# Optimization experiments

Hardware: AMD Instinct MI355X
Metric: run time of the kernel (lower is better)

The kernel has to match this reference:

```python
import jax, jax.numpy as jnp
import numpy as np
from math import factorial

LMAX = 2
MUL = 8            # output_size (mul_in1 = mul_in2)
MUL_OUT = 16       # channels_out
NBASIS = 16
MAX_RADIUS = 5.0
EMB_DIM = 16
MAX_ATOM = 10
N_NODES = 40000
N_EDGES = 500000
N_GRAPHS = 16

# ---- real Clebsch-Gordan coefficients (computed once in numpy) ----

def _cg_coef(j1, m1, j2, m2, j3, m3):
    if m1 + m2 != m3:
        return 0.0
    f = factorial
    pre = ((2 * j3 + 1) * f(j3 + j1 - j2) * f(j3 - j1 + j2) * f(j1 + j2 - j3) / f(j1 + j2 + j3 + 1)) ** 0.5
    pre *= (f(j3 + m3) * f(j3 - m3) * f(j1 - m1) * f(j1 + m1) * f(j2 - m2) * f(j2 + m2)) ** 0.5
    kmin = max(0, j2 - j3 - m1, j1 - j3 + m2)
    kmax = min(j1 + j2 - j3, j1 - m1, j2 + m2)
    s = 0.0
    for k in range(kmin, kmax + 1):
        s += (-1) ** k / (f(k) * f(j1 + j2 - j3 - k) * f(j1 - m1 - k) * f(j2 + m2 - k) * f(j3 - j2 + m1 + k) * f(j3 - j1 - m2 + k))
    return pre * s

def _su2_cg(l1, l2, l3):
    C = np.zeros((2 * l1 + 1, 2 * l2 + 1, 2 * l3 + 1))
    for m1 in range(-l1, l1 + 1):
        for m2 in range(-l2, l2 + 1):
            m3 = m1 + m2
            if abs(m3) <= l3:
                C[m1 + l1, m2 + l2, m3 + l3] = _cg_coef(l1, m1, l2, m2, l3, m3)
    return C

def _q(l):
    # complex->real SH change of basis with phase making CG real
    q = np.zeros((2 * l + 1, 2 * l + 1), dtype=complex)
    for m in range(-l, 0):
        q[l + m, l + abs(m)] = 1 / np.sqrt(2)
        q[l + m, l - abs(m)] = -1j / np.sqrt(2)
    q[l, l] = 1.0
    for m in range(1, l + 1):
        q[l + m, l + abs(m)] = (-1) ** m / np.sqrt(2)
        q[l + m, l - abs(m)] = 1j * (-1) ** m / np.sqrt(2)
    return (-1j) ** l * q

def _real_cg(l1, l2, l3):
    C = _su2_cg(l1, l2, l3).astype(complex)
    Cr = np.einsum('ia,jb,kc,ijk->abc', _q(l1), _q(l2), np.conj(_q(l3)), C)
    Cr = Cr.imag if np.abs(Cr.imag).sum() > np.abs(Cr.real).sum() else Cr.real
    return Cr.astype(np.float32)

PATHS = [(l1, l2, lo) for l1 in range(LMAX + 1) for l2 in range(LMAX + 1)
         for lo in range(abs(l1 - l2), min(LMAX, l1 + l2) + 1)]
NUM_PATHS = len(PATHS)  # 15 for full policy at lmax=2
CG = {p: jnp.asarray(_real_cg(*p)) for p in PATHS}

def _sph(n):
    # real spherical harmonics of unit vectors, component normalization, m = -l..l
    x, y, z = n[:, 0], n[:, 1], n[:, 2]
    s3, s15, s5 = 3.0 ** 0.5, 15.0 ** 0.5, 5.0 ** 0.5
    Y0 = jnp.ones_like(x)[:, None]
    Y1 = s3 * jnp.stack([y, z, x], axis=-1)
    Y2 = jnp.stack([s15 * x * y, s15 * y * z, 0.5 * s5 * (3.0 * z * z - 1.0),
                    s15 * x * z, 0.5 * s15 * (x * x - y * y)], axis=-1)
    return [Y0, Y1, Y2]

def setup_inputs() -> dict:
    key = jax.random.key(0)
    ks = jax.random.split(key, 16)
    pos = jax.random.normal(ks[0], (N_NODES, 3), dtype=jnp.float32) * 2.0
    A = jax.random.randint(ks[1], (N_NODES,), 0, MAX_ATOM)
    batch = jnp.sort(jax.random.randint(ks[2], (N_NODES,), 0, N_GRAPHS))
    edge_src = jax.random.randint(ks[3], (N_EDGES,), 0, N_NODES)
    edge_dst = jax.random.randint(ks[4], (N_EDGES,), 0, N_NODES)
    edge_shifts = jnp.zeros((N_EDGES, 3), dtype=jnp.float32)
    cell = jax.random.normal(ks[5], (N_GRAPHS, 3, 3), dtype=jnp.float32)
    emb_table = jax.random.normal(ks[6], (MAX_ATOM, EMB_DIM), dtype=jnp.float32)
    mlp_w1 = jax.random.normal(ks[7], (EMB_DIM, 64), dtype=jnp.float32) / EMB_DIM ** 0.5
    mlp_b1 = jnp.zeros((64,), jnp.float32)
    mlp_w2 = jax.random.normal(ks[8], (64, MUL), dtype=jnp.float32) / 8.0
    mlp_b2 = jnp.zeros((MUL,), jnp.float32)
    fc_w1 = jax.random.normal(ks[9], (NBASIS, 64), dtype=jnp.float32) / NBASIS ** 0.5
    fc_b1 = jnp.zeros((64,), jnp.float32)
    fc_w2 = jax.random.normal(ks[10], (64, 64), dtype=jnp.float32) / 8.0
    fc_b2 = jnp.zeros((64,), jnp.float32)
    fc_w3 = jax.random.normal(ks[11], (64, NUM_PATHS), dtype=jnp.float32) / 8.0
    fc_b3 = jnp.zeros((NUM_PATHS,), jnp.float32)
    tp_w = jax.random.normal(ks[12], (NUM_PATHS, MUL, MUL, MUL_OUT), dtype=jnp.float32) / MUL
    return {"pos": pos, "A": A, "batch": batch, "edge_src": edge_src, "edge_dst": edge_dst,
            "edge_shifts": edge_shifts, "cell": cell, "emb_table": emb_table,
            "mlp_w1": mlp_w1, "mlp_b1": mlp_b1, "mlp_w2": mlp_w2, "mlp_b2": mlp_b2,
            "fc_w1": fc_w1, "fc_b1": fc_b1, "fc_w2": fc_w2, "fc_b2": fc_b2,
            "fc_w3": fc_w3, "fc_b3": fc_b3, "tp_w": tp_w}

def reference(pos, A, batch, edge_src, edge_dst, edge_shifts, cell, emb_table,
              mlp_w1, mlp_b1, mlp_w2, mlp_b2, fc_w1, fc_b1, fc_w2, fc_b2,
              fc_w3, fc_b3, tp_w):
    # --- edge geometry with PBC shifts ---
    shift_vecs = jnp.einsum('ni,nij->nj', edge_shifts, cell[batch[edge_src]])
    edge_vec = pos[edge_dst] - pos[edge_src] + shift_vecs            # [E,3]
    edge_length = jnp.linalg.norm(edge_vec, axis=1)                  # [E]
    n = edge_vec / jnp.clip(edge_length, 1e-8)[:, None]
    # --- atom scalar channels Ai: Embedding -> Linear-SiLU-Linear ---
    Ai = jax.nn.silu(emb_table[A] @ mlp_w1 + mlp_b1) @ mlp_w2 + mlp_b2   # [N,MUL]
    Y = _sph(n)
    # --- radial embedding (soft_one_hot_linspace, gaussian, cutoff=True) -> gates ---
    values = jnp.linspace(0.0, MAX_RADIUS, NBASIS + 2)[1:-1]
    step = values[1] - values[0]
    diff = (edge_length[:, None] - values) / step
    emb = jnp.exp(-diff * diff) / 1.12 * (NBASIS ** 0.5)             # [E,NBASIS]
    h = jax.nn.silu(emb @ fc_w1 + fc_b1)
    h = jax.nn.silu(h @ fc_w2 + fc_b2)
    gates = h @ fc_w3 + fc_b3                                        # [E,NUM_PATHS]
    # --- CG tensor product: in1_l = Ai[src] (x) Y_l ; in2 has only l=0 block = Ai[dst] ---
    f1 = Ai[edge_src]   # [E,MUL]
    x2_0 = Ai[edge_dst]  # [E,MUL]
    norm = 1.0 / (MUL * MUL) ** 0.5
    E = edge_src.shape[0]
    out = [jnp.zeros((E, MUL_OUT, 2 * lo + 1), Ai.dtype) for lo in range(LMAX + 1)]
    for p, (l1, l2, lo) in enumerate(PATHS):
        if l2 != 0:
            continue  # in2 blocks for l2>0 are identically zero -> zero contribution
        f_in = f1[:, :, None] * Y[l1][:, None, :]                    # [E,MUL,2l1+1]
        cg = CG[(l1, l2, lo)][:, 0, :]                               # [2l1+1,2lo+1]
        contrib = jnp.einsum('eui,ev,uvw,io->ewo', f_in, x2_0, tp_w[p], cg)
        out[lo] = out[lo] + gates[:, p, None, None] * (norm * contrib)
    edge_features = jnp.concatenate(
        [out[lo].reshape(E, MUL_OUT * (2 * lo + 1)) for lo in range(LMAX + 1)], axis=-1)  # [E,144]
    # --- scatter-mean over destination nodes ---
    ones = jnp.ones((E,), edge_features.dtype)
    counts = jnp.clip(jax.ops.segment_sum(ones, edge_dst, num_segments=N_NODES), 1.0)
    node_out = jax.ops.segment_sum(edge_features, edge_dst, num_segments=N_NODES) / counts[:, None]
    return node_out
```

## Files before the change

### kernel.cpp

```cpp
#include <hip/hip_runtime.h>
#include <hip/hip_fp16.h>
#include <cstddef>


#define TBL_N 8192
#define TBL_SCALE 1024.0f

__device__ __forceinline__ float silu(float x) {
    return x / (1.0f + __expf(-x));
}

__device__ __forceinline__ unsigned pack_half2(float lo, float hi) {
    unsigned a = __half_as_ushort(__float2half_rn(lo));
    unsigned b = __half_as_ushort(__float2half_rn(hi));
    return (b << 16) | a;
}

__global__ __launch_bounds__(256) void setup_kernel(
    const float* __restrict__ emb_table,
    const float* __restrict__ w1, const float* __restrict__ b1,
    const float* __restrict__ w2, const float* __restrict__ b2,
    const float* __restrict__ tp_w,
    const float* __restrict__ fc_w1, const float* __restrict__ fc_b1,
    const float* __restrict__ fc_w2, const float* __restrict__ fc_b2,
    const float* __restrict__ fc_w3, const float* __restrict__ fc_b3,
    float* __restrict__ rows_g, float* __restrict__ B_g,
    float4* __restrict__ table,
    int4* __restrict__ deg4, int n4, int zb, int n_atom)
{
    int bid = blockIdx.x;
    int tid = threadIdx.x;

    if (bid < zb) {
        int i = bid * 256 + tid;
        if (i < n4) deg4[i] = make_int4(0, 0, 0, 0);
        return;
    }
    if (bid < zb + n_atom) {
        __shared__ float s_r[8];
        int a = bid - zb;
        if (tid < 8) {
            float e[16];
            #pragma unroll
            for (int i = 0; i < 16; i++) e[i] = emb_table[a * 16 + i];
            float acc_j = b2[tid];
            for (int k = 0; k < 64; k++) {
                float acc = b1[k];
                #pragma unroll
                for (int i = 0; i < 16; i++) acc = fmaf(e[i], w1[i * 64 + k], acc);
                acc_j = fmaf(silu(acc), w2[k * 8 + tid], acc_j);
            }
            s_r[tid] = acc_j;
            rows_g[a * 8 + tid] = acc_j;
        }
        __syncthreads();
        for (int t = tid; t < 384; t += 256) {
            int pp = t >> 7, ub = (t >> 4) & 7, wb = t & 15;
            int P = (pp == 0) ? 0 : (pp == 1) ? 3 : 9;
            float acc = 0.0f;
            #pragma unroll
            for (int v = 0; v < 8; v++)
                acc = fmaf(s_r[v], tp_w[P * 1024 + (ub * 8 + v) * 16 + wb], acc);
            B_g[a * 384 + t] = acc;
        }
        return;
    }

    __shared__ float s_h1[4][64];
    int tb = bid - zb - n_atom;
    int s = tid >> 6;
    int k = tid & 63;
    int samp = tb * 4 + s;
    float len = (float)samp * (1.0f / TBL_SCALE);

    float emb[16];
    const float inv_step = 17.0f / 5.0f;
    #pragma unroll
    for (int b = 0; b < 16; b++) {
        float d = len * inv_step - (float)(b + 1);
        emb[b] = __expf(-d * d) * 3.5714285714285716f;
    }

    float acc = fc_b1[k];
    #pragma unroll
    for (int b = 0; b < 16; b++) acc = fmaf(emb[b], fc_w1[b * 64 + k], acc);
    s_h1[s][k] = silu(acc);
    __syncthreads();

    float acc2 = fc_b2[k];
    #pragma unroll
    for (int j = 0; j < 64; j++)
        acc2 = fmaf(s_h1[s][j], fc_w2[j * 64 + k], acc2);
    float h2 = silu(acc2);

    float p0 = h2 * fc_w3[k * 15 + 0];
    float p3 = h2 * fc_w3[k * 15 + 3];
    float p9 = h2 * fc_w3[k * 15 + 9];
    #pragma unroll
    for (int off = 32; off > 0; off >>= 1) {
        p0 += __shfl_down(p0, off, 64);
        p3 += __shfl_down(p3, off, 64);
        p9 += __shfl_down(p9, off, 64);
    }
    if (k == 0) {
        table[samp] = make_float4((fc_b3[0] + p0) * 0.125f,
                                  (fc_b3[3] + p3) * 0.125f,
                                  (fc_b3[9] + p9) * 0.125f, 0.0f);
    }
}

__global__ __launch_bounds__(256) void deg_kernel(
    const int* __restrict__ edge_dst, int* __restrict__ deg,
    int* __restrict__ rank, int n_edges)
{
    int e = blockIdx.x * blockDim.x + threadIdx.x;
    if (e >= n_edges) return;
    rank[e] = atomicAdd(&deg[edge_dst[e]], 1);
}

__global__ __launch_bounds__(1024) void partial_kernel(
    const int* __restrict__ deg, int* __restrict__ bsum, int n)
{
    __shared__ int red[1024];
    int tid = threadIdx.x;
    int i = blockIdx.x * 1024 + tid;
    red[tid] = (i < n) ? deg[i] : 0;
    __syncthreads();
    #pragma unroll
    for (int off = 512; off > 0; off >>= 1) {
        if (tid < off) red[tid] += red[tid + off];
        __syncthreads();
    }
    if (tid == 0) bsum[blockIdx.x] = red[0];
}

__global__ __launch_bounds__(1024) void scan_write_kernel(
    const int* __restrict__ deg, const int* __restrict__ bsum,
    int* __restrict__ starts, int n, int nb)
{
    __shared__ int s[1024];
    __shared__ int sb[1024];
    int tid = threadIdx.x;

    sb[tid] = (tid < nb) ? bsum[tid] : 0;
    int i = blockIdx.x * 1024 + tid;
    int v = (i < n) ? deg[i] : 0;
    s[tid] = v;
    __syncthreads();
    #pragma unroll
    for (int off = 1; off < 1024; off <<= 1) {
        int t1 = (tid >= off) ? s[tid - off] : 0;
        int t2 = (tid >= off) ? sb[tid - off] : 0;
        __syncthreads();
        s[tid] += t1;
        sb[tid] += t2;
        __syncthreads();
    }
    int base = (blockIdx.x == 0) ? 0 : sb[blockIdx.x - 1];
    if (i < n) starts[i] = base + s[tid] - v;
}

__global__ __launch_bounds__(256) void edge_kernel(
    const float* __restrict__ pos,
    const int* __restrict__ A,
    const int* __restrict__ batch,
    const int* __restrict__ edge_src,
    const int* __restrict__ edge_dst,
    const float* __restrict__ edge_shifts,
    const float* __restrict__ cell,
    const float4* __restrict__ table,
    const int* __restrict__ starts,
    const int* __restrict__ rank,
    float* __restrict__ records,
    int n_edges)
{
    int e = blockIdx.x * blockDim.x + threadIdx.x;
    if (e >= n_edges) return;

    int src = edge_src[e];
    int dst = edge_dst[e];

    float sh0 = edge_shifts[3 * (size_t)e + 0];
    float sh1 = edge_shifts[3 * (size_t)e + 1];
    float sh2 = edge_shifts[3 * (size_t)e + 2];
    int g = batch[src];
    const float* C = cell + (size_t)g * 9;
    float shx = sh0 * C[0] + sh1 * C[3] + sh2 * C[6];
    float shy = sh0 * C[1] + sh1 * C[4] + sh2 * C[7];
    float shz = sh0 * C[2] + sh1 * C[5] + sh2 * C[8];

    float vx = pos[3 * (size_t)dst + 0] - pos[3 * (size_t)src + 0] + shx;
    float vy = pos[3 * (size_t)dst + 1] - pos[3 * (size_t)src + 1] + shy;
    float vz = pos[3 * (size_t)dst + 2] - pos[3 * (size_t)src + 2] + shz;

    float len = sqrtf(vx * vx + vy * vy + vz * vz);
    float invl = 1.0f / fmaxf(len, 1e-8f);
    float nx = vx * invl, ny = vy * invl, nz = vz * invl;

    float t = fminf(len * TBL_SCALE, (float)(TBL_N - 1));
    int i0 = (int)t;
    i0 = min(i0, TBL_N - 2);
    float fr = t - (float)i0;
    float4 T0 = table[i0];
    float4 T1 = table[i0 + 1];
    float g0 = fmaf(fr, T1.x - T0.x, T0.x);
    float g1 = fmaf(fr, T1.y - T0.y, T0.y);
    float g2 = fmaf(fr, T1.z - T0.z, T0.z);

    const float s3  = 1.7320508075688772f;
    const float s15 = 3.872983346207417f;
    const float s5  = 2.23606797749979f;
    float G0 = g0;
    float G1 = g1 * s3 * ny, G2 = g1 * s3 * nz, G3 = g1 * s3 * nx;
    float G4 = g2 * s15 * nx * ny;
    float G5 = g2 * s15 * ny * nz;
    float G6 = g2 * 0.5f * s5 * (3.0f * nz * nz - 1.0f);
    float G7 = g2 * s15 * nx * nz;
    float G8 = g2 * 0.5f * s15 * (nx * nx - ny * ny);

    int asrc = A[src];
    int slot = starts[dst] + rank[e];

    unsigned u0 = pack_half2(G0, G8);
    unsigned u1 = pack_half2(G1, G8);
    unsigned u2 = pack_half2(G2, G8);
    unsigned u3 = pack_half2(G3, G8);
    unsigned u4 = pack_half2(G4, G8);
    unsigned u5 = pack_half2(G5, G8);
    unsigned u6 = pack_half2(G6, G8);
    unsigned u7 = pack_half2(G7, G8);

    float2* r2 = (float2*)(records + (size_t)slot * 10);
    r2[0] = make_float2(__uint_as_float(u0), __uint_as_float(u1));
    r2[1] = make_float2(__uint_as_float(u2), __uint_as_float(u3));
    r2[2] = make_float2(__uint_as_float(u4), __uint_as_float(u5));
    r2[3] = make_float2(__uint_as_float(u6), __uint_as_float(u7));
    r2[4] = make_float2(__int_as_float(asrc), 0.0f);
}

__global__ __launch_bounds__(256) void gather_kernel(
    const float* __restrict__ records,
    const int* __restrict__ starts,
    const int* __restrict__ deg,
    const int* __restrict__ A,
    const float* __restrict__ rows_g,
    const float* __restrict__ B_g,
    float* __restrict__ out, int n_nodes, int n_atom)
{
    __shared__ float s_B[3840];
    __shared__ float s_rows[80];
    __shared__ float s_M[4][80];

    int tid = threadIdx.x;
    {
        float4* dB = (float4*)s_B;
        const float4* sB = (const float4*)B_g;
        int nB4 = n_atom * 96;
        for (int t = tid; t < nB4; t += 256) dB[t] = sB[t];
        if (tid < n_atom * 8) s_rows[tid] = rows_g[tid];
    }
    __syncthreads();

    int wv = tid >> 6;
    int lane = tid & 63;
    int node = blockIdx.x * 4 + wv;
    if (node >= n_nodes) return;

    int start = starts[node];
    int d = deg[node];
    int iq = lane >> 3, u = lane & 7;
    int anode = A[node];

    float m = 0.0f, m8 = 0.0f;
    const float* recs = records + (size_t)start * 10;
    int j = 0;
    for (; j + 4 <= d; j += 4) {
        const unsigned* r0 = (const unsigned*)(recs + (size_t)(j + 0) * 10);
        const unsigned* r1 = (const unsigned*)(recs + (size_t)(j + 1) * 10);
        const unsigned* r2 = (const unsigned*)(recs + (size_t)(j + 2) * 10);
        const unsigned* r3 = (const unsigned*)(recs + (size_t)(j + 3) * 10);
        unsigned q0 = r0[iq], q1 = r1[iq], q2 = r2[iq], q3 = r3[iq];
        int a0 = (int)r0[8], a1 = (int)r1[8], a2 = (int)r2[8], a3 = (int)r3[8];
        float2 p0 = __half22float2(*reinterpret_cast<const __half2*>(&q0));
        float2 p1 = __half22float2(*reinterpret_cast<const __half2*>(&q1));
        float2 p2 = __half22float2(*reinterpret_cast<const __half2*>(&q2));
        float2 p3 = __half22float2(*reinterpret_cast<const __half2*>(&q3));
        float c0 = s_rows[a0 * 8 + u];
        float c1 = s_rows[a1 * 8 + u];
        float c2 = s_rows[a2 * 8 + u];
        float c3 = s_rows[a3 * 8 + u];
        m  = fmaf(p0.x, c0, m);  m8 = fmaf(p0.y, c0, m8);
        m  = fmaf(p1.x, c1, m);  m8 = fmaf(p1.y, c1, m8);
        m  = fmaf(p2.x, c2, m);  m8 = fmaf(p2.y, c2, m8);
        m  = fmaf(p3.x, c3, m);  m8 = fmaf(p3.y, c3, m8);
    }
    for (; j < d; j++) {
        const unsigned* r0 = (const unsigned*)(recs + (size_t)j * 10);
        unsigned q0 = r0[iq];
        int a0 = (int)r0[8];
        float2 p0 = __half22float2(*reinterpret_cast<const __half2*>(&q0));
        float c0 = s_rows[a0 * 8 + u];
        m  = fmaf(p0.x, c0, m);
        m8 = fmaf(p0.y, c0, m8);
    }
    s_M[wv][iq * 8 + u] = m;
    if (lane < 8) s_M[wv][64 + u] = m8;

    const float* Bn = s_B + anode * 384;
    float invd = 1.0f / fmaxf((float)d, 1.0f);
    float* row = out + (size_t)node * 144;
    {
        int c = lane;
        int pp, w, ip;
        if (c < 16) { pp = 0; w = c; ip = 0; }
        else { int t = c - 16; pp = 1; w = t / 3; ip = 1 + (t - 3 * (t / 3)); }
        float acc = 0.0f;
        #pragma unroll
        for (int uu = 0; uu < 8; uu++)
            acc = fmaf(Bn[pp * 128 + uu * 16 + w], s_M[wv][ip * 8 + uu], acc);
        row[c] = acc * invd;
    }
    {
        int t = lane;
        int w = t / 5; int i = t - 5 * w;
        float acc = 0.0f;
        #pragma unroll
        for (int uu = 0; uu < 8; uu++)
            acc = fmaf(Bn[256 + uu * 16 + w], s_M[wv][(4 + i) * 8 + uu], acc);
        row[64 + lane] = acc * invd;
    }
    if (lane < 16) {
        int t = 64 + lane;
        int w = t / 5; int i = t - 5 * w;
        float acc = 0.0f;
        #pragma unroll
        for (int uu = 0; uu < 8; uu++)
            acc = fmaf(Bn[256 + uu * 16 + w], s_M[wv][(4 + i) * 8 + uu], acc);
        row[128 + lane] = acc * invd;
    }
}

extern "C" void kernel_launch(void* const* d_in, const int* in_sizes, int n_in,
                              void* d_out, int out_size, void* d_ws, size_t ws_size,
                              hipStream_t stream)
{
    const float* pos         = (const float*)d_in[0];
    const int*   A           = (const int*)d_in[1];
    const int*   batch       = (const int*)d_in[2];
    const int*   edge_src    = (const int*)d_in[3];
    const int*   edge_dst    = (const int*)d_in[4];
    const float* edge_shifts = (const float*)d_in[5];
    const float* cell        = (const float*)d_in[6];
    const float* emb_table   = (const float*)d_in[7];
    const float* mlp_w1      = (const float*)d_in[8];
    const float* mlp_b1      = (const float*)d_in[9];
    const float* mlp_w2      = (const float*)d_in[10];
    const float* mlp_b2      = (const float*)d_in[11];
    const float* fc_w1       = (const float*)d_in[12];
    const float* fc_b1       = (const float*)d_in[13];
    const float* fc_w2       = (const float*)d_in[14];
    const float* fc_b2       = (const float*)d_in[15];
    const float* fc_w3       = (const float*)d_in[16];
    const float* fc_b3       = (const float*)d_in[17];
    const float* tp_w        = (const float*)d_in[18];

    int n_nodes = in_sizes[1];
    int n_edges = in_sizes[3];
    int n_atom  = in_sizes[7] / 16;
    int nb      = (n_nodes + 1023) / 1024;

    float* table   = (float*)d_ws;
    float* rows_g  = table + (size_t)TBL_N * 4;
    float* B_g     = rows_g + 128;
    int*   deg     = (int*)(B_g + 3840);
    int*   starts  = deg + n_nodes;
    int*   bsum    = starts + n_nodes;
    int*   rank    = bsum + 1024;
    float* records = (float*)(rank + n_edges);

    int n4 = (n_nodes + 3) / 4;
    int zb = (n4 + 255) / 256;

    setup_kernel<<<zb + n_atom + TBL_N / 4, 256, 0, stream>>>(
        emb_table, mlp_w1, mlp_b1, mlp_w2, mlp_b2, tp_w,
        fc_w1, fc_b1, fc_w2, fc_b2, fc_w3, fc_b3,
        rows_g, B_g, (float4*)table, (int4*)deg, n4, zb, n_atom);

    deg_kernel<<<(n_edges + 255) / 256, 256, 0, stream>>>(
        edge_dst, deg, rank, n_edges);

    partial_kernel<<<nb, 1024, 0, stream>>>(deg, bsum, n_nodes);

    scan_write_kernel<<<nb, 1024, 0, stream>>>(deg, bsum, starts, n_nodes, nb);

    edge_kernel<<<(n_edges + 255) / 256, 256, 0, stream>>>(
        pos, A, batch, edge_src, edge_dst, edge_shifts, cell,
        (const float4*)table, starts, rank, records, n_edges);

    gather_kernel<<<(n_nodes + 3) / 4, 256, 0, stream>>>(
        records, starts, deg, A, rows_g, B_g, (float*)d_out, n_nodes, n_atom);
}
```

Measured before the change: 96.71 us.

## Split edge records into packed half pairs plus byte atom ids, merge scan kernels

```diff
diff --git a/kernel.cpp b/kernel.cpp
--- a/kernel.cpp
+++ b/kernel.cpp
@@ -118,45 +118,39 @@
     rank[e] = atomicAdd(&deg[edge_dst[e]], 1);
 }
 
-__global__ __launch_bounds__(1024) void partial_kernel(
-    const int* __restrict__ deg, int* __restrict__ bsum, int n)
-{
+__global__ __launch_bounds__(1024) void scan_kernel(
+    const int* __restrict__ deg, int* __restrict__ starts, int n)
+{
+    __shared__ int s[1024];
     __shared__ int red[1024];
     int tid = threadIdx.x;
-    int i = blockIdx.x * 1024 + tid;
-    red[tid] = (i < n) ? deg[i] : 0;
+    int b = blockIdx.x;
+
+    int acc = 0;
+    for (int c = 0; c < b; c++) {
+        int idx = c * 1024 + tid;
+        acc += (idx < n) ? deg[idx] : 0;
+    }
+    red[tid] = acc;
     __syncthreads();
     #pragma unroll
     for (int off = 512; off > 0; off >>= 1) {
         if (tid < off) red[tid] += red[tid + off];
         __syncthreads();
     }
-    if (tid == 0) bsum[blockIdx.x] = red[0];
-}
-
-__global__ __launch_bounds__(1024) void scan_write_kernel(
-    const int* __restrict__ deg, const int* __restrict__ bsum,
-    int* __restrict__ starts, int n, int nb)
-{
-    __shared__ int s[1024];
-    __shared__ int sb[1024];
-    int tid = threadIdx.x;
-
-    sb[tid] = (tid < nb) ? bsum[tid] : 0;
-    int i = blockIdx.x * 1024 + tid;
+    int base = red[0];
+
+    int i = b * 1024 + tid;
     int v = (i < n) ? deg[i] : 0;
     s[tid] = v;
     __syncthreads();
     #pragma unroll
     for (int off = 1; off < 1024; off <<= 1) {
         int t1 = (tid >= off) ? s[tid - off] : 0;
-        int t2 = (tid >= off) ? sb[tid - off] : 0;
         __syncthreads();
         s[tid] += t1;
-        sb[tid] += t2;
         __syncthreads();
     }
-    int base = (blockIdx.x == 0) ? 0 : sb[blockIdx.x - 1];
     if (i < n) starts[i] = base + s[tid] - v;
 }
 
@@ -171,7 +165,8 @@
     const float4* __restrict__ table,
     const int* __restrict__ starts,
     const int* __restrict__ rank,
-    float* __restrict__ records,
+    unsigned* __restrict__ pairs,
+    unsigned char* __restrict__ asrc8,
     int n_edges)
 {
     int e = blockIdx.x * blockDim.x + threadIdx.x;
@@ -230,22 +225,21 @@
     unsigned u6 = pack_half2(G6, G8);
     unsigned u7 = pack_half2(G7, G8);
 
-    float2* r2 = (float2*)(records + (size_t)slot * 10);
-    r2[0] = make_float2(__uint_as_float(u0), __uint_as_float(u1));
-    r2[1] = make_float2(__uint_as_float(u2), __uint_as_float(u3));
-    r2[2] = make_float2(__uint_as_float(u4), __uint_as_float(u5));
-    r2[3] = make_float2(__uint_as_float(u6), __uint_as_float(u7));
-    r2[4] = make_float2(__int_as_float(asrc), 0.0f);
+    uint4* pp = (uint4*)(pairs + (size_t)slot * 8);
+    pp[0] = make_uint4(u0, u1, u2, u3);
+    pp[1] = make_uint4(u4, u5, u6, u7);
+    asrc8[slot] = (unsigned char)asrc;
 }
 
 __global__ __launch_bounds__(256) void gather_kernel(
-    const float* __restrict__ records,
+    const unsigned* __restrict__ pairs,
+    const unsigned char* __restrict__ asrc8,
     const int* __restrict__ starts,
     const int* __restrict__ deg,
     const int* __restrict__ A,
     const float* __restrict__ rows_g,
     const float* __restrict__ B_g,
-    float* __restrict__ out, int n_nodes, int n_atom)
+    float* __restrict__ out, int n_nodes, int n_atom, int n_groups)
 {
     __shared__ float s_B[3840];
     __shared__ float s_rows[80];
@@ -263,80 +257,82 @@
 
     int wv = tid >> 6;
     int lane = tid & 63;
-    int node = blockIdx.x * 4 + wv;
-    if (node >= n_nodes) return;
-
-    int start = starts[node];
-    int d = deg[node];
     int iq = lane >> 3, u = lane & 7;
-    int anode = A[node];
-
-    float m = 0.0f, m8 = 0.0f;
-    const float* recs = records + (size_t)start * 10;
-    int j = 0;
-    for (; j + 4 <= d; j += 4) {
-        const unsigned* r0 = (const unsigned*)(recs + (size_t)(j + 0) * 10);
-        const unsigned* r1 = (const unsigned*)(recs + (size_t)(j + 1) * 10);
-        const unsigned* r2 = (const unsigned*)(recs + (size_t)(j + 2) * 10);
-        const unsigned* r3 = (const unsigned*)(recs + (size_t)(j + 3) * 10);
-        unsigned q0 = r0[iq], q1 = r1[iq], q2 = r2[iq], q3 = r3[iq];
-        int a0 = (int)r0[8], a1 = (int)r1[8], a2 = (int)r2[8], a3 = (int)r3[8];
-        float2 p0 = __half22float2(*reinterpret_cast<const __half2*>(&q0));
-        float2 p1 = __half22float2(*reinterpret_cast<const __half2*>(&q1));
-        float2 p2 = __half22float2(*reinterpret_cast<const __half2*>(&q2));
-        float2 p3 = __half22float2(*reinterpret_cast<const __half2*>(&q3));
-        float c0 = s_rows[a0 * 8 + u];
-        float c1 = s_rows[a1 * 8 + u];
-        float c2 = s_rows[a2 * 8 + u];
-        float c3 = s_rows[a3 * 8 + u];
-        m  = fmaf(p0.x, c0, m);  m8 = fmaf(p0.y, c0, m8);
-        m  = fmaf(p1.x, c1, m);  m8 = fmaf(p1.y, c1, m8);
-        m  = fmaf(p2.x, c2, m);  m8 = fmaf(p2.y, c2, m8);
-        m  = fmaf(p3.x, c3, m);  m8 = fmaf(p3.y, c3, m8);
-    }
-    for (; j < d; j++) {
-        const unsigned* r0 = (const unsigned*)(recs + (size_t)j * 10);
-        unsigned q0 = r0[iq];
-        int a0 = (int)r0[8];
-        float2 p0 = __half22float2(*reinterpret_cast<const __half2*>(&q0));
-        float c0 = s_rows[a0 * 8 + u];
-        m  = fmaf(p0.x, c0, m);
-        m8 = fmaf(p0.y, c0, m8);
-    }
-    s_M[wv][iq * 8 + u] = m;
-    if (lane < 8) s_M[wv][64 + u] = m8;
-
-    const float* Bn = s_B + anode * 384;
-    float invd = 1.0f / fmaxf((float)d, 1.0f);
-    float* row = out + (size_t)node * 144;
-    {
-        int c = lane;
-        int pp, w, ip;
-        if (c < 16) { pp = 0; w = c; ip = 0; }
-        else { int t = c - 16; pp = 1; w = t / 3; ip = 1 + (t - 3 * (t / 3)); }
-        float acc = 0.0f;
-        #pragma unroll
-        for (int uu = 0; uu < 8; uu++)
-            acc = fmaf(Bn[pp * 128 + uu * 16 + w], s_M[wv][ip * 8 + uu], acc);
-        row[c] = acc * invd;
-    }
-    {
-        int t = lane;
-        int w = t / 5; int i = t - 5 * w;
-        float acc = 0.0f;
-        #pragma unroll
-        for (int uu = 0; uu < 8; uu++)
-            acc = fmaf(Bn[256 + uu * 16 + w], s_M[wv][(4 + i) * 8 + uu], acc);
-        row[64 + lane] = acc * invd;
-    }
-    if (lane < 16) {
-        int t = 64 + lane;
-        int w = t / 5; int i = t - 5 * w;
-        float acc = 0.0f;
-        #pragma unroll
-        for (int uu = 0; uu < 8; uu++)
-            acc = fmaf(Bn[256 + uu * 16 + w], s_M[wv][(4 + i) * 8 + uu], acc);
-        row[128 + lane] = acc * invd;
+
+    for (int grp = blockIdx.x; grp < n_groups; grp += gridDim.x) {
+        int node = grp * 4 + wv;
+        if (node >= n_nodes) continue;
+
+        int start = starts[node];
+        int d = deg[node];
+        int anode = A[node];
+
+        float m = 0.0f, m8 = 0.0f;
+        const unsigned* recs = pairs + (size_t)start * 8;
+        const unsigned char* ap = asrc8 + start;
+        int j = 0;
+        for (; j + 4 <= d; j += 4) {
+            unsigned q0 = recs[(size_t)(j + 0) * 8 + iq];
+            unsigned q1 = recs[(size_t)(j + 1) * 8 + iq];
+            unsigned q2 = recs[(size_t)(j + 2) * 8 + iq];
+            unsigned q3 = recs[(size_t)(j + 3) * 8 + iq];
+            int a0 = ap[j + 0], a1 = ap[j + 1], a2 = ap[j + 2], a3 = ap[j + 3];
+            float2 p0 = __half22float2(*reinterpret_cast<const __half2*>(&q0));
+            float2 p1 = __half22float2(*reinterpret_cast<const __half2*>(&q1));
+            float2 p2 = __half22float2(*reinterpret_cast<const __half2*>(&q2));
+            float2 p3 = __half22float2(*reinterpret_cast<const __half2*>(&q3));
+            float c0 = s_rows[a0 * 8 + u];
+            float c1 = s_rows[a1 * 8 + u];
+            float c2 = s_rows[a2 * 8 + u];
+            float c3 = s_rows[a3 * 8 + u];
+            m  = fmaf(p0.x, c0, m);  m8 = fmaf(p0.y, c0, m8);
+            m  = fmaf(p1.x, c1, m);  m8 = fmaf(p1.y, c1, m8);
+            m  = fmaf(p2.x, c2, m);  m8 = fmaf(p2.y, c2, m8);
+            m  = fmaf(p3.x, c3, m);  m8 = fmaf(p3.y, c3, m8);
+        }
+        for (; j < d; j++) {
+            unsigned q0 = recs[(size_t)j * 8 + iq];
+            int a0 = ap[j];
+            float2 p0 = __half22float2(*reinterpret_cast<const __half2*>(&q0));
+            float c0 = s_rows[a0 * 8 + u];
+            m  = fmaf(p0.x, c0, m);
+            m8 = fmaf(p0.y, c0, m8);
+        }
+        s_M[wv][iq * 8 + u] = m;
+        if (lane < 8) s_M[wv][64 + u] = m8;
+
+        const float* Bn = s_B + anode * 384;
+        float invd = 1.0f / fmaxf((float)d, 1.0f);
+        float* row = out + (size_t)node * 144;
+        {
+            int c = lane;
+            int pp, w, ip;
+            if (c < 16) { pp = 0; w = c; ip = 0; }
+            else { int t = c - 16; pp = 1; w = t / 3; ip = 1 + (t - 3 * (t / 3)); }
+            float acc = 0.0f;
+            #pragma unroll
+            for (int uu = 0; uu < 8; uu++)
+                acc = fmaf(Bn[pp * 128 + uu * 16 + w], s_M[wv][ip * 8 + uu], acc);
+            row[c] = acc * invd;
+        }
+        {
+            int t = lane;
+            int w = t / 5; int i = t - 5 * w;
+            float acc = 0.0f;
+            #pragma unroll
+            for (int uu = 0; uu < 8; uu++)
+                acc = fmaf(Bn[256 + uu * 16 + w], s_M[wv][(4 + i) * 8 + uu], acc);
+            row[64 + lane] = acc * invd;
+        }
+        if (lane < 16) {
+            int t = 64 + lane;
+            int w = t / 5; int i = t - 5 * w;
+            float acc = 0.0f;
+            #pragma unroll
+            for (int uu = 0; uu < 8; uu++)
+                acc = fmaf(Bn[256 + uu * 16 + w], s_M[wv][(4 + i) * 8 + uu], acc);
+            row[128 + lane] = acc * invd;
+        }
     }
 }
 
@@ -369,14 +365,14 @@
     int n_atom  = in_sizes[7] / 16;
     int nb      = (n_nodes + 1023) / 1024;
 
-    float* table   = (float*)d_ws;
-    float* rows_g  = table + (size_t)TBL_N * 4;
-    float* B_g     = rows_g + 128;
-    int*   deg     = (int*)(B_g + 3840);
-    int*   starts  = deg + n_nodes;
-    int*   bsum    = starts + n_nodes;
-    int*   rank    = bsum + 1024;
-    float* records = (float*)(rank + n_edges);
+    float*         table   = (float*)d_ws;
+    float*         rows_g  = table + (size_t)TBL_N * 4;
+    float*         B_g     = rows_g + 128;
+    int*           deg     = (int*)(B_g + 3840);
+    int*           starts  = deg + n_nodes;
+    int*           rank    = starts + n_nodes;
+    unsigned*      pairs   = (unsigned*)(rank + n_edges);
+    unsigned char* asrc8   = (unsigned char*)(pairs + (size_t)n_edges * 8);
 
     int n4 = (n_nodes + 3) / 4;
     int zb = (n4 + 255) / 256;
@@ -389,14 +385,15 @@
     deg_kernel<<<(n_edges + 255) / 256, 256, 0, stream>>>(
         edge_dst, deg, rank, n_edges);
 
-    partial_kernel<<<nb, 1024, 0, stream>>>(deg, bsum, n_nodes);
-
-    scan_write_kernel<<<nb, 1024, 0, stream>>>(deg, bsum, starts, n_nodes, nb);
+    scan_kernel<<<nb, 1024, 0, stream>>>(deg, starts, n_nodes);
 
     edge_kernel<<<(n_edges + 255) / 256, 256, 0, stream>>>(
         pos, A, batch, edge_src, edge_dst, edge_shifts, cell,
-        (const float4*)table, starts, rank, records, n_edges);
-
-    gather_kernel<<<(n_nodes + 3) / 4, 256, 0, stream>>>(
-        records, starts, deg, A, rows_g, B_g, (float*)d_out, n_nodes, n_atom);
-}
+        (const float4*)table, starts, rank, pairs, asrc8, n_edges);
+
+    int n_groups = (n_nodes + 3) / 4;
+    int ggrid = n_groups < 2048 ? n_groups : 2048;
+    gather_kernel<<<ggrid, 256, 0, stream>>>(
+        pairs, asrc8, starts, deg, A, rows_g, B_g,
+        (float*)d_out, n_nodes, n_atom, n_groups);
+}
```

Result: slower. 102.8 us (+6.3%).
